# Performance work log

Measured on AMD Instinct MI355X. Metric: run time of the kernel, lower is better.

The kernel has to match this reference:

```python
import jax, jax.numpy as jnp
import numpy as np

IN_DIM, OUT_DIM, EDGE_DIM = 128, 64, 16
BS, N = 8, 512

def setup_inputs() -> dict:
    key = jax.random.key(0)
    k1, k2, k3, k4 = jax.random.split(key, 4)
    x = jax.random.normal(k1, (BS, N, IN_DIM), dtype=jnp.float32)
    edge_feats = jax.random.normal(k2, (BS, N, N, EDGE_DIM), dtype=jnp.float32)
    # nn.Linear weights: fc (out_dim, in_dim), attn_fc (1, 2*out_dim+edge_dim)
    W_fc = jax.random.normal(k3, (OUT_DIM, IN_DIM), dtype=jnp.float32) / np.sqrt(IN_DIM)
    attn_w = jax.random.normal(k4, (2 * OUT_DIM + EDGE_DIM,), dtype=jnp.float32) / np.sqrt(2 * OUT_DIM + EDGE_DIM)
    return {"x": x, "edge_feats": edge_feats, "W_fc": W_fc, "attn_w": attn_w}

def reference(x, edge_feats, W_fc, attn_w):
    # h: (bs, N, out_dim)
    h = jnp.einsum('bni,oi->bno', x, W_fc)
    # Split attn_fc weight: concat([h_i, h_j, edge]) @ a == h_i@a_i + h_j@a_j + edge@a_e
    a_i = attn_w[:OUT_DIM]
    a_j = attn_w[OUT_DIM:2 * OUT_DIM]
    a_e = attn_w[2 * OUT_DIM:]
    s_i = jnp.einsum('bno,o->bn', h, a_i)              # (bs, N)
    s_j = jnp.einsum('bno,o->bn', h, a_j)              # (bs, N)
    s_e = jnp.einsum('bijk,k->bij', edge_feats, a_e)   # (bs, N, N)
    e_ij = s_i[:, :, None] + s_j[:, None, :] + s_e     # (bs, N, N)
    alpha = jax.nn.softmax(e_ij, axis=-1)              # softmax over j
    # weighted sum of h_j over j
    h_prime = jnp.einsum('bij,bjo->bio', alpha, h)
    return h_prime
```

## Files before the change

### kernel.cpp

```cpp
#include <hip/hip_runtime.h>

constexpr int IN_DIM = 128;
constexpr int OUT_DIM = 64;
constexpr int EDGE_DIM = 16;
constexpr int BS = 8;
constexpr int NN = 512;
constexpr int ROWS = BS * NN;

__global__ __launch_bounds__(256, 2) void fc_kernel(
    const float* __restrict__ x, const float* __restrict__ W,
    const float* __restrict__ attn_w,
    float* __restrict__ h, float* __restrict__ si, float* __restrict__ sj)
{
    __shared__ float xs[16 * IN_DIM];
    const int t    = threadIdx.x;
    const int lane = t & 63;
    const int w    = t >> 6;
    const int rowBase = blockIdx.x * 16;

    const float4* x4 = (const float4*)(x + (size_t)rowBase * IN_DIM);
    float4* xs4 = (float4*)xs;
    xs4[t]       = x4[t];
    xs4[t + 256] = x4[t + 256];

    const float a_i = attn_w[lane];
    const float a_j = attn_w[OUT_DIM + lane];
    __syncthreads();

    const float4* W4 = (const float4*)W;
    float acc[4] = {0.f, 0.f, 0.f, 0.f};
    #pragma unroll 8
    for (int k = 0; k < IN_DIM / 4; ++k) {
        float4 wv = W4[lane * (IN_DIM / 4) + k];
        #pragma unroll
        for (int r = 0; r < 4; ++r) {
            float4 xv = ((const float4*)&xs[(w * 4 + r) * IN_DIM])[k];
            acc[r] += xv.x * wv.x + xv.y * wv.y + xv.z * wv.z + xv.w * wv.w;
        }
    }
    #pragma unroll
    for (int r = 0; r < 4; ++r) {
        const int row = rowBase + w * 4 + r;
        h[(size_t)row * OUT_DIM + lane] = acc[r];
        float pi = acc[r] * a_i;
        float pj = acc[r] * a_j;
        #pragma unroll
        for (int off = 32; off > 0; off >>= 1) {
            pi += __shfl_down(pi, off, 64);
            pj += __shfl_down(pj, off, 64);
        }
        if (lane == 0) { si[row] = pi; sj[row] = pj; }
    }
}

__global__ __launch_bounds__(256, 4) void attn_kernel(
    const float* __restrict__ edge, const float* __restrict__ attn_w,
    const float* __restrict__ h, const float* __restrict__ si,
    const float* __restrict__ sj, float* __restrict__ out)
{
    __shared__ float alpha[NN];
    __shared__ float redm[4];
    __shared__ float reds[4];
    __shared__ float4 part[16][16];

    const int t    = threadIdx.x;
    const int lane = t & 63;
    const int w    = t >> 6;
    const int blk  = blockIdx.x;
    const int b    = blk >> 9;

    const float4* ae4 = (const float4*)(attn_w + 2 * OUT_DIM);
    const float4 ae0 = ae4[0], ae1 = ae4[1], ae2 = ae4[2], ae3 = ae4[3];
    const float  siv = si[blk];
    const float4* ef4 = (const float4*)edge + (size_t)blk * NN * EDGE_DIM / 4;
    const float* sjb  = sj + (b << 9);

    float e0, e1;
    {
        int j = t;
        float4 v0 = ef4[j * 4 + 0], v1 = ef4[j * 4 + 1];
        float4 v2 = ef4[j * 4 + 2], v3 = ef4[j * 4 + 3];
        float se = v0.x * ae0.x + v0.y * ae0.y + v0.z * ae0.z + v0.w * ae0.w
                 + v1.x * ae1.x + v1.y * ae1.y + v1.z * ae1.z + v1.w * ae1.w
                 + v2.x * ae2.x + v2.y * ae2.y + v2.z * ae2.z + v2.w * ae2.w
                 + v3.x * ae3.x + v3.y * ae3.y + v3.z * ae3.z + v3.w * ae3.w;
        e0 = siv + sjb[j] + se;
        j = t + 256;
        v0 = ef4[j * 4 + 0]; v1 = ef4[j * 4 + 1];
        v2 = ef4[j * 4 + 2]; v3 = ef4[j * 4 + 3];
        se = v0.x * ae0.x + v0.y * ae0.y + v0.z * ae0.z + v0.w * ae0.w
           + v1.x * ae1.x + v1.y * ae1.y + v1.z * ae1.z + v1.w * ae1.w
           + v2.x * ae2.x + v2.y * ae2.y + v2.z * ae2.z + v2.w * ae2.w
           + v3.x * ae3.x + v3.y * ae3.y + v3.z * ae3.z + v3.w * ae3.w;
        e1 = siv + sjb[j] + se;
    }

    float m = fmaxf(e0, e1);
    #pragma unroll
    for (int off = 32; off > 0; off >>= 1) m = fmaxf(m, __shfl_down(m, off, 64));
    if (lane == 0) redm[w] = m;
    __syncthreads();
    m = fmaxf(fmaxf(redm[0], redm[1]), fmaxf(redm[2], redm[3]));

    const float p0 = __expf(e0 - m);
    const float p1 = __expf(e1 - m);
    alpha[t]       = p0;
    alpha[t + 256] = p1;
    float s = p0 + p1;
    #pragma unroll
    for (int off = 32; off > 0; off >>= 1) s += __shfl_down(s, off, 64);
    if (lane == 0) reds[w] = s;
    __syncthreads();
    const float rinv = 1.0f / (reds[0] + reds[1] + reds[2] + reds[3]);

    const int o4 = t & 15;
    const int g  = t >> 4;
    const float4* h4 = (const float4*)(h + ((size_t)(b << 9)) * OUT_DIM);
    float4 acc = {0.f, 0.f, 0.f, 0.f};
    #pragma unroll 4
    for (int j = g; j < NN; j += 16) {
        const float a  = alpha[j];
        const float4 hv = h4[j * 16 + o4];
        acc.x += a * hv.x; acc.y += a * hv.y;
        acc.z += a * hv.z; acc.w += a * hv.w;
    }
    part[g][o4] = acc;
    __syncthreads();
    if (t < 16) {
        float4 r = part[0][t];
        #pragma unroll
        for (int g2 = 1; g2 < 16; ++g2) {
            const float4 p = part[g2][t];
            r.x += p.x; r.y += p.y; r.z += p.z; r.w += p.w;
        }
        r.x *= rinv; r.y *= rinv; r.z *= rinv; r.w *= rinv;
        ((float4*)out)[(size_t)blk * 16 + t] = r;
    }
}

extern "C" void kernel_launch(void* const* d_in, const int* in_sizes, int n_in,
                              void* d_out, int out_size, void* d_ws, size_t ws_size,
                              hipStream_t stream) {
    const float* x      = (const float*)d_in[0];
    const float* edge   = (const float*)d_in[1];
    const float* W_fc   = (const float*)d_in[2];
    const float* attn_w = (const float*)d_in[3];
    float* out = (float*)d_out;

    float* h  = (float*)d_ws;
    float* si = h + (size_t)ROWS * OUT_DIM;
    float* sj = si + ROWS;

    fc_kernel<<<ROWS / 16, 256, 0, stream>>>(x, W_fc, attn_w, h, si, sj);
    attn_kernel<<<ROWS, 256, 0, stream>>>(edge, attn_w, h, si, sj, out);
}
```

Baseline: 212.9 us.

## Process four query rows per attention block, one wave per row softmax

The attention kernel now handles four query rows per block, with each wave computing one row's edge scores and softmax entirely through wave shuffles, so the cross-wave shared-memory reductions and one barrier go away. Each h_j value loaded in the aggregation loop is reused across the four rows, cutting h reads from L2 by four. The fc kernel is retiled to eight rows per block with more blocks. The trade-off is fewer blocks, more registers per thread, and an edge-read pattern in which each wave streams a single row.

```diff
diff --git a/kernel.cpp b/kernel.cpp
--- a/kernel.cpp
+++ b/kernel.cpp
@@ -6,48 +6,48 @@
 constexpr int BS = 8;
 constexpr int NN = 512;
 constexpr int ROWS = BS * NN;
+constexpr int TI = 4;
 
-__global__ __launch_bounds__(256, 2) void fc_kernel(
+__global__ __launch_bounds__(256, 4) void fc_kernel(
     const float* __restrict__ x, const float* __restrict__ W,
     const float* __restrict__ attn_w,
     float* __restrict__ h, float* __restrict__ si, float* __restrict__ sj)
 {
-    __shared__ float xs[16 * IN_DIM];
+    __shared__ float xs[8 * IN_DIM];
     const int t    = threadIdx.x;
     const int lane = t & 63;
     const int w    = t >> 6;
-    const int rowBase = blockIdx.x * 16;
+    const int rowBase = blockIdx.x * 8;
 
-    const float4* x4 = (const float4*)(x + (size_t)rowBase * IN_DIM);
-    float4* xs4 = (float4*)xs;
-    xs4[t]       = x4[t];
-    xs4[t + 256] = x4[t + 256];
+    ((float4*)xs)[t] = ((const float4*)(x + (size_t)rowBase * IN_DIM))[t];
 
     const float a_i = attn_w[lane];
     const float a_j = attn_w[OUT_DIM + lane];
     __syncthreads();
 
     const float4* W4 = (const float4*)W;
-    float acc[4] = {0.f, 0.f, 0.f, 0.f};
+    float acc0 = 0.f, acc1 = 0.f;
+    const float4* xr0 = (const float4*)&xs[(w * 2 + 0) * IN_DIM];
+    const float4* xr1 = (const float4*)&xs[(w * 2 + 1) * IN_DIM];
     #pragma unroll 8
     for (int k = 0; k < IN_DIM / 4; ++k) {
-        float4 wv = W4[lane * (IN_DIM / 4) + k];
-        #pragma unroll
-        for (int r = 0; r < 4; ++r) {
-            float4 xv = ((const float4*)&xs[(w * 4 + r) * IN_DIM])[k];
-            acc[r] += xv.x * wv.x + xv.y * wv.y + xv.z * wv.z + xv.w * wv.w;
-        }
+        const float4 wv = W4[lane * (IN_DIM / 4) + k];
+        const float4 x0 = xr0[k];
+        const float4 x1 = xr1[k];
+        acc0 += x0.x * wv.x + x0.y * wv.y + x0.z * wv.z + x0.w * wv.w;
+        acc1 += x1.x * wv.x + x1.y * wv.y + x1.z * wv.z + x1.w * wv.w;
     }
     #pragma unroll
-    for (int r = 0; r < 4; ++r) {
-        const int row = rowBase + w * 4 + r;
-        h[(size_t)row * OUT_DIM + lane] = acc[r];
-        float pi = acc[r] * a_i;
-        float pj = acc[r] * a_j;
+    for (int r = 0; r < 2; ++r) {
+        const float a   = r ? acc1 : acc0;
+        const int   row = rowBase + w * 2 + r;
+        h[(size_t)row * OUT_DIM + lane] = a;
+        float pi = a * a_i;
+        float pj = a * a_j;
         #pragma unroll
-        for (int off = 32; off > 0; off >>= 1) {
-            pi += __shfl_down(pi, off, 64);
-            pj += __shfl_down(pj, off, 64);
+        for (int m = 32; m > 0; m >>= 1) {
+            pi += __shfl_xor(pi, m, 64);
+            pj += __shfl_xor(pj, m, 64);
         }
         if (lane == 0) { si[row] = pi; sj[row] = pj; }
     }
@@ -58,83 +58,83 @@
     const float* __restrict__ h, const float* __restrict__ si,
     const float* __restrict__ sj, float* __restrict__ out)
 {
-    __shared__ float alpha[NN];
-    __shared__ float redm[4];
-    __shared__ float reds[4];
-    __shared__ float4 part[16][16];
+    __shared__ float  alpha[TI * NN];
+    __shared__ float4 part[TI][16][16];
 
     const int t    = threadIdx.x;
     const int lane = t & 63;
     const int w    = t >> 6;
     const int blk  = blockIdx.x;
-    const int b    = blk >> 9;
+    const int b    = blk >> 7;
+    const int iRow = (blk & 127) * TI + w;
+    const int rowg = (b << 9) + iRow;
 
     const float4* ae4 = (const float4*)(attn_w + 2 * OUT_DIM);
     const float4 ae0 = ae4[0], ae1 = ae4[1], ae2 = ae4[2], ae3 = ae4[3];
-    const float  siv = si[blk];
-    const float4* ef4 = (const float4*)edge + (size_t)blk * NN * EDGE_DIM / 4;
+    const float  siv = si[rowg];
+    const float4* ef4 = (const float4*)edge + (size_t)rowg * NN * EDGE_DIM / 4;
     const float* sjb  = sj + (b << 9);
 
-    float e0, e1;
-    {
-        int j = t;
-        float4 v0 = ef4[j * 4 + 0], v1 = ef4[j * 4 + 1];
-        float4 v2 = ef4[j * 4 + 2], v3 = ef4[j * 4 + 3];
-        float se = v0.x * ae0.x + v0.y * ae0.y + v0.z * ae0.z + v0.w * ae0.w
-                 + v1.x * ae1.x + v1.y * ae1.y + v1.z * ae1.z + v1.w * ae1.w
-                 + v2.x * ae2.x + v2.y * ae2.y + v2.z * ae2.z + v2.w * ae2.w
-                 + v3.x * ae3.x + v3.y * ae3.y + v3.z * ae3.z + v3.w * ae3.w;
-        e0 = siv + sjb[j] + se;
-        j = t + 256;
-        v0 = ef4[j * 4 + 0]; v1 = ef4[j * 4 + 1];
-        v2 = ef4[j * 4 + 2]; v3 = ef4[j * 4 + 3];
-        se = v0.x * ae0.x + v0.y * ae0.y + v0.z * ae0.z + v0.w * ae0.w
-           + v1.x * ae1.x + v1.y * ae1.y + v1.z * ae1.z + v1.w * ae1.w
-           + v2.x * ae2.x + v2.y * ae2.y + v2.z * ae2.z + v2.w * ae2.w
-           + v3.x * ae3.x + v3.y * ae3.y + v3.z * ae3.z + v3.w * ae3.w;
-        e1 = siv + sjb[j] + se;
+    float e[8];
+    #pragma unroll 2
+    for (int jj = 0; jj < 8; ++jj) {
+        const int j = jj * 64 + lane;
+        const float4 v0 = ef4[j * 4 + 0], v1 = ef4[j * 4 + 1];
+        const float4 v2 = ef4[j * 4 + 2], v3 = ef4[j * 4 + 3];
+        const float se = v0.x * ae0.x + v0.y * ae0.y + v0.z * ae0.z + v0.w * ae0.w
+                       + v1.x * ae1.x + v1.y * ae1.y + v1.z * ae1.z + v1.w * ae1.w
+                       + v2.x * ae2.x + v2.y * ae2.y + v2.z * ae2.z + v2.w * ae2.w
+                       + v3.x * ae3.x + v3.y * ae3.y + v3.z * ae3.z + v3.w * ae3.w;
+        e[jj] = siv + sjb[j] + se;
     }
 
-    float m = fmaxf(e0, e1);
+    float m = e[0];
     #pragma unroll
-    for (int off = 32; off > 0; off >>= 1) m = fmaxf(m, __shfl_down(m, off, 64));
-    if (lane == 0) redm[w] = m;
+    for (int jj = 1; jj < 8; ++jj) m = fmaxf(m, e[jj]);
+    #pragma unroll
+    for (int msk = 32; msk > 0; msk >>= 1) m = fmaxf(m, __shfl_xor(m, msk, 64));
+
+    float p[8], s = 0.f;
+    #pragma unroll
+    for (int jj = 0; jj < 8; ++jj) { p[jj] = __expf(e[jj] - m); s += p[jj]; }
+    #pragma unroll
+    for (int msk = 32; msk > 0; msk >>= 1) s += __shfl_xor(s, msk, 64);
+    const float rinv = 1.0f / s;
+    #pragma unroll
+    for (int jj = 0; jj < 8; ++jj)
+        alpha[w * NN + jj * 64 + lane] = p[jj] * rinv;
+
     __syncthreads();
-    m = fmaxf(fmaxf(redm[0], redm[1]), fmaxf(redm[2], redm[3]));
-
-    const float p0 = __expf(e0 - m);
-    const float p1 = __expf(e1 - m);
-    alpha[t]       = p0;
-    alpha[t + 256] = p1;
-    float s = p0 + p1;
-    #pragma unroll
-    for (int off = 32; off > 0; off >>= 1) s += __shfl_down(s, off, 64);
-    if (lane == 0) reds[w] = s;
-    __syncthreads();
-    const float rinv = 1.0f / (reds[0] + reds[1] + reds[2] + reds[3]);
 
     const int o4 = t & 15;
     const int g  = t >> 4;
     const float4* h4 = (const float4*)(h + ((size_t)(b << 9)) * OUT_DIM);
-    float4 acc = {0.f, 0.f, 0.f, 0.f};
+    float4 acc[TI];
+    #pragma unroll
+    for (int r = 0; r < TI; ++r) acc[r] = make_float4(0.f, 0.f, 0.f, 0.f);
     #pragma unroll 4
     for (int j = g; j < NN; j += 16) {
-        const float a  = alpha[j];
         const float4 hv = h4[j * 16 + o4];
-        acc.x += a * hv.x; acc.y += a * hv.y;
-        acc.z += a * hv.z; acc.w += a * hv.w;
+        #pragma unroll
+        for (int r = 0; r < TI; ++r) {
+            const float a = alpha[r * NN + j];
+            acc[r].x += a * hv.x; acc[r].y += a * hv.y;
+            acc[r].z += a * hv.z; acc[r].w += a * hv.w;
+        }
     }
-    part[g][o4] = acc;
+    #pragma unroll
+    for (int r = 0; r < TI; ++r) part[r][g][o4] = acc[r];
     __syncthreads();
-    if (t < 16) {
-        float4 r = part[0][t];
+
+    if (t < 64) {
+        const int r = t >> 4, c = t & 15;
+        float4 v = part[r][0][c];
         #pragma unroll
         for (int g2 = 1; g2 < 16; ++g2) {
-            const float4 p = part[g2][t];
-            r.x += p.x; r.y += p.y; r.z += p.z; r.w += p.w;
+            const float4 q = part[r][g2][c];
+            v.x += q.x; v.y += q.y; v.z += q.z; v.w += q.w;
         }
-        r.x *= rinv; r.y *= rinv; r.z *= rinv; r.w *= rinv;
-        ((float4*)out)[(size_t)blk * 16 + t] = r;
+        ((float4*)out)[((size_t)(b << 9) + (blk & 127) * TI + r) * 16 + c] = v;
     }
 }
 
@@ -151,6 +151,6 @@
     float* si = h + (size_t)ROWS * OUT_DIM;
     float* sj = si + ROWS;
 
-    fc_kernel<<<ROWS / 16, 256, 0, stream>>>(x, W_fc, attn_w, h, si, sj);
-    attn_kernel<<<ROWS, 256, 0, stream>>>(edge, attn_w, h, si, sj, out);
+    fc_kernel<<<ROWS / 8, 256, 0, stream>>>(x, W_fc, attn_w, h, si, sj);
+    attn_kernel<<<ROWS / TI, 256, 0, stream>>>(edge, attn_w, h, si, sj, out);
 }
```

Measured after the change: 210.3 us. No clear change (-1.2%).
